# Optimization experiments

Hardware: AMD Instinct MI355X
Metric: run time of the kernel (lower is better)

## Reference

```python
import jax, jax.numpy as jnp
import numpy as np

N_FEAT = 1024
NEG_BIG = -1e30  # finite stand-in for -inf to avoid NaNs on fully-masked rows


def setup_inputs() -> dict:
    key = jax.random.key(0)
    k1, k2, k3 = jax.random.split(key, 3)
    T, C = 4096, 1024
    x = jax.random.normal(k1, (T, C), dtype=jnp.float32)
    W = jax.random.normal(k2, (C, 3 * N_FEAT), dtype=jnp.float32) * 0.02
    b = jax.random.normal(k3, (3 * N_FEAT,), dtype=jnp.float32) * 0.02
    return {"x": x, "W": W, "b": b, "n_padd": 256}


def reference(x, W, b, n_padd):
    T, C = x.shape
    qkv = x @ W + b  # [T, 3*N_FEAT]
    q, k, v = jnp.split(qkv, 3, axis=1)  # each [T, N_FEAT]
    att = (q @ k.T) * (1.0 / jnp.sqrt(jnp.float32(N_FEAT)))  # [T, T]
    idx = jnp.arange(T)
    causal = idx[None, :] <= idx[:, None]
    data = (idx[None, :] >= n_padd) & (idx[:, None] >= n_padd)
    mask = causal & data
    att = jnp.where(mask, att, NEG_BIG)
    p = jax.nn.softmax(att, axis=-1)  # fully-masked rows -> uniform, zeroed below
    y = p @ v  # [T, N_FEAT]
    # kernel only stores rows >= n_padd; padded rows defined as zero here
    y = jnp.where(idx[:, None] >= n_padd, y, 0.0)
    return y
```

## Files before the change

kernel.cpp:

```cpp
#include <hip/hip_runtime.h>
#include <hip/hip_bf16.h>
#include <stdint.h>
#include <stddef.h>

#define TT 4096
#define CC 1024
#define NFD 1024
#define N3 3072
#define PB0 1152
#define PB2 2176

typedef __bf16 bf16;
typedef __bf16 bf16x8 __attribute__((ext_vector_type(8)));
typedef __bf16 bf16x4 __attribute__((ext_vector_type(4)));
typedef float f32x4 __attribute__((ext_vector_type(4)));

typedef const __attribute__((address_space(1))) unsigned char gl_u8;
typedef __attribute__((address_space(3))) unsigned char lds_u8;

__device__ __forceinline__ void glds16(const void* g, void* l) {
  __builtin_amdgcn_global_load_lds((gl_u8*)g, (lds_u8*)l, 16, 0, 0);
}

__device__ __forceinline__ void stage128x32(const bf16* __restrict__ src, int ld, bf16* lds, int tid) {
  const int lane = tid & 63;
  const int w = tid >> 6;
#pragma unroll
  for (int p = 0; p < 2; ++p) {
    const int lbyte = w * 2048 + p * 1024;
    const int row = (lbyte >> 6) + (lane >> 2);
    const int kel = (lane & 3) << 3;
    glds16(src + row * ld + kel, (char*)lds + lbyte);
  }
}

__device__ __forceinline__ void gemm_core(const bf16* __restrict__ A, const bf16* __restrict__ B,
                                          int lda, int ldb, int ksteps,
                                          bf16* As, bf16* Bs, int tid, f32x4 (&acc)[4][4]) {
  const int lane = tid & 63;
  const int w = tid >> 6;
  const int wm = (w >> 1) * 64;
  const int wn = (w & 1) * 64;
  const int lrow = lane & 15;
  const int lko = (lane >> 4) * 8;
  stage128x32(A, lda, As, tid);
  stage128x32(B, ldb, Bs, tid);
  __syncthreads();
  for (int ks = 0; ks < ksteps; ++ks) {
    const bf16* Ac = As + (ks & 1) * 4096;
    const bf16* Bc = Bs + (ks & 1) * 4096;
    if (ks + 1 < ksteps) {
      stage128x32(A + (ks + 1) * 32, lda, As + ((ks + 1) & 1) * 4096, tid);
      stage128x32(B + (ks + 1) * 32, ldb, Bs + ((ks + 1) & 1) * 4096, tid);
    }
    bf16x8 af[4], bfr[4];
#pragma unroll
    for (int i = 0; i < 4; ++i)
      af[i] = *(const bf16x8*)(Ac + (wm + i * 16 + lrow) * 32 + lko);
#pragma unroll
    for (int i = 0; i < 4; ++i)
      bfr[i] = *(const bf16x8*)(Bc + (wn + i * 16 + lrow) * 32 + lko);
#pragma unroll
    for (int mi = 0; mi < 4; ++mi)
#pragma unroll
      for (int ni = 0; ni < 4; ++ni)
        acc[mi][ni] = __builtin_amdgcn_mfma_f32_16x16x32_bf16(af[mi], bfr[ni], acc[mi][ni], 0, 0, 0);
    __syncthreads();
  }
}

__global__ __launch_bounds__(256) void k_prep(const float* __restrict__ x, bf16* __restrict__ xb,
                                              const float* __restrict__ Wsrc, bf16* __restrict__ WbT,
                                              float* __restrict__ l) {
  __shared__ float Ls[64][65];
  const int tid = threadIdx.x;
  if (blockIdx.x < 2048) {
    int idx = (blockIdx.x * 256 + tid) * 8;
    f32x4 a = *(const f32x4*)(x + idx);
    f32x4 b = *(const f32x4*)(x + idx + 4);
    bf16x8 o;
#pragma unroll
    for (int j = 0; j < 4; ++j) { o[j] = (bf16)a[j]; o[4 + j] = (bf16)b[j]; }
    *(bf16x8*)(xb + idx) = o;
    return;
  }
  if (blockIdx.x == 2048 + 768) {
    f32x4 z = (f32x4){0.f, 0.f, 0.f, 0.f};
#pragma unroll
    for (int qq = 0; qq < 4; ++qq)
      *(f32x4*)(l + (qq * 256 + tid) * 4) = z;
    return;
  }
  const int bid = blockIdx.x - 2048;
  const int n0 = (bid % 48) * 64;
  const int c0 = (bid / 48) * 64;
#pragma unroll
  for (int qq = 0; qq < 4; ++qq) {
    int lin = qq * 1024 + tid * 4;
    int r = lin >> 6, cc = lin & 63;
    f32x4 v = *(const f32x4*)(Wsrc + (size_t)(c0 + r) * N3 + n0 + cc);
#pragma unroll
    for (int j = 0; j < 4; ++j) Ls[r][cc + j] = v[j];
  }
  __syncthreads();
#pragma unroll
  for (int qq = 0; qq < 4; ++qq) {
    int lin = qq * 1024 + tid * 4;
    int nr = lin >> 6, cc = lin & 63;
    bf16x4 o;
#pragma unroll
    for (int j = 0; j < 4; ++j) o[j] = (bf16)Ls[cc + j][nr];
    *(bf16x4*)(WbT + (size_t)(n0 + nr) * CC + c0 + cc) = o;
  }
}

__global__ __launch_bounds__(256, 2) void k_qkv(const bf16* __restrict__ xb, const bf16* __restrict__ wbt,
                                                const float* __restrict__ bias,
                                                bf16* __restrict__ q, bf16* __restrict__ k,
                                                bf16* __restrict__ vT) {
  __shared__ bf16 As[2 * 128 * 32], Bs[2 * 128 * 32];
  const int tid = threadIdx.x;
  const int id = blockIdx.x;
  const int r = id & 7;
  const int s = id >> 3;
  const int it = 4 * r + (s & 3);
  const int jt = s >> 2;
  const int m0 = it * 128;
  const int n0 = jt * 128;
  f32x4 acc[4][4];
#pragma unroll
  for (int i = 0; i < 4; ++i)
#pragma unroll
    for (int j = 0; j < 4; ++j) acc[i][j] = (f32x4){0.f, 0.f, 0.f, 0.f};

  gemm_core(xb + (size_t)m0 * CC, wbt + (size_t)n0 * CC, CC, CC, CC / 32, As, Bs, tid, acc);

  const int lane = tid & 63;
  const int w = tid >> 6;
  const int wm = (w >> 1) * 64, wn = (w & 1) * 64;
  const int seg = n0 >> 10;
#pragma unroll
  for (int mi = 0; mi < 4; ++mi) {
    const int tB = m0 + wm + mi * 16 + ((lane >> 4) << 2);
#pragma unroll
    for (int ni = 0; ni < 4; ++ni) {
      const int n = n0 + wn + ni * 16 + (lane & 15);
      const float bb = bias[n];
      f32x4 a = acc[mi][ni];
      if (seg == 2) {
        bf16x4 pv;
#pragma unroll
        for (int r2 = 0; r2 < 4; ++r2) pv[r2] = (bf16)(a[r2] + bb);
        *(bf16x4*)(vT + (size_t)(n - 2048) * TT + tB) = pv;
      } else {
        bf16* dst = (seg == 0) ? q : k;
        const int nl = n & 1023;
#pragma unroll
        for (int r2 = 0; r2 < 4; ++r2) dst[(size_t)(tB + r2) * NFD + nl] = (bf16)(a[r2] + bb);
      }
    }
  }
}

__global__ __launch_bounds__(256, 2) void k_scores(const bf16* __restrict__ q, const bf16* __restrict__ kk,
                                                   bf16* __restrict__ P, float* __restrict__ l,
                                                   const int* __restrict__ npadd_p) {
  const int id = blockIdx.x;
  const int lin = (id & 7) * 66 + (id >> 3);
  int band, rem;
  if (lin < 228)      { band = 0; rem = lin; }
  else if (lin < 392) { band = 1; rem = lin - 228; }
  else if (lin < 492) { band = 2; rem = lin - 392; }
  else                { band = 3; rem = lin - 492; }
  int it, jt;
  if (rem < 28) {
    int itp = (int)((sqrtf(8.0f * (float)rem + 1.0f) - 1.0f) * 0.5f);
    while ((itp + 1) * (itp + 2) / 2 <= rem) ++itp;
    while (itp * (itp + 1) / 2 > rem) --itp;
    it = band * 8 + itp;
    jt = band * 8 + (rem - itp * (itp + 1) / 2);
  } else {
    const int rem2 = rem - 28;
    it = band * 8 + 7 + (rem2 >> 3);
    jt = band * 8 + (rem2 & 7);
  }
  const int np = *npadd_p;
  const int jt0 = np >> 7;
  if (jt < jt0) return;

  __shared__ bf16 As[2 * 128 * 32], Bs[2 * 128 * 32];
  const int tid = threadIdx.x;
  f32x4 acc[4][4];
#pragma unroll
  for (int i = 0; i < 4; ++i)
#pragma unroll
    for (int j = 0; j < 4; ++j) acc[i][j] = (f32x4){0.f, 0.f, 0.f, 0.f};

  gemm_core(q + (size_t)it * 128 * CC, kk + (size_t)jt * 128 * CC, CC, CC, CC / 32, As, Bs, tid, acc);

  const int lane = tid & 63;
  const int w = tid >> 6;
  const int wm = (w >> 1) * 64, wn = (w & 1) * 64;
  const float scale = 0.03125f;
#pragma unroll
  for (int mi = 0; mi < 4; ++mi) {
    const int iB = it * 128 + wm + mi * 16 + ((lane >> 4) << 2);
    float rs[4] = {0.f, 0.f, 0.f, 0.f};
#pragma unroll
    for (int ni = 0; ni < 4; ++ni) {
      const int j = jt * 128 + wn + ni * 16 + (lane & 15);
      f32x4 a = acc[mi][ni];
#pragma unroll
      for (int r = 0; r < 4; ++r) {
        const int i = iB + r;
        float p = 0.f;
        if (j <= i && j >= np && i >= np) p = __expf(a[r] * scale);
        const bf16 pb = (bf16)p;
        P[(size_t)i * TT + j] = pb;
        rs[r] += (float)pb;
      }
    }
#pragma unroll
    for (int r = 0; r < 4; ++r) {
      float v = rs[r];
      v += __shfl_xor(v, 1);
      v += __shfl_xor(v, 2);
      v += __shfl_xor(v, 4);
      v += __shfl_xor(v, 8);
      if ((lane & 15) == 0) atomicAdd(&l[iB + r], v);
    }
  }
}

__global__ __launch_bounds__(256, 2) void k_pvc(const bf16* __restrict__ P, const bf16* __restrict__ vT,
                                                bf16* __restrict__ part0, bf16* __restrict__ part1,
                                                bf16* __restrict__ part2,
                                                const float* __restrict__ l, float* __restrict__ y,
                                                const int* __restrict__ npadd_p) {
  const int id = blockIdx.x;
  const int kgrp = id >> 3;
  const int d0 = (kgrp & 7) * 128;
  const int p = (id & 7) + 8 * (kgrp >> 3);
  const int it = p >> 2;
  const int c = p & 3;
  const int np = *npadd_p;
  const int jt0 = np >> 7;
  const int lo = (c == 0) ? 0 : (c == 1 ? 9 : (c == 2 ? 17 : 25));
  const int hi = (c == 0) ? 9 : (c == 1 ? 17 : (c == 2 ? 25 : 32));
  const int jlo = max(lo, jt0);
  const int jhi = min(hi, it + 1);
  if (jlo >= jhi) return;

  __shared__ bf16 As[2 * 128 * 32], Bs[2 * 128 * 32];
  const int tid = threadIdx.x;
  f32x4 acc[4][4];
#pragma unroll
  for (int i = 0; i < 4; ++i)
#pragma unroll
    for (int j = 0; j < 4; ++j) acc[i][j] = (f32x4){0.f, 0.f, 0.f, 0.f};

  gemm_core(P + (size_t)it * 128 * TT + (size_t)jlo * 128,
            vT + (size_t)d0 * TT + (size_t)jlo * 128,
            TT, TT, (jhi - jlo) * 4, As, Bs, tid, acc);

  const int lane = tid & 63;
  const int w = tid >> 6;
  const int wm = (w >> 1) * 64, wn = (w & 1) * 64;
  const bool sole = (jlo == jt0) && (jhi == it + 1);
  if (sole) {
#pragma unroll
    for (int mi = 0; mi < 4; ++mi) {
      const int iB = it * 128 + wm + mi * 16 + ((lane >> 4) << 2);
      float inv4[4];
#pragma unroll
      for (int r = 0; r < 4; ++r) {
        const int i = iB + r;
        inv4[r] = (i >= np) ? (1.0f / l[i]) : 0.0f;
      }
#pragma unroll
      for (int ni = 0; ni < 4; ++ni) {
        const int d = d0 + wn + ni * 16 + (lane & 15);
        f32x4 a = acc[mi][ni];
#pragma unroll
        for (int r = 0; r < 4; ++r)
          y[(size_t)(iB + r) * NFD + d] = a[r] * inv4[r];
      }
    }
  } else if (c == 3) {
#pragma unroll
    for (int mi = 0; mi < 4; ++mi) {
      const int iB = it * 128 + wm + mi * 16 + ((lane >> 4) << 2);
#pragma unroll
      for (int ni = 0; ni < 4; ++ni) {
        const int d = d0 + wn + ni * 16 + (lane & 15);
        f32x4 a = acc[mi][ni];
#pragma unroll
        for (int r = 0; r < 4; ++r)
          y[(size_t)(iB + r) * NFD + d] = a[r];
      }
    }
  } else {
    bf16* __restrict__ part = (c == 0) ? part0 : (c == 1 ? part1 : part2);
    const int base = (c == 2) ? (PB2 * NFD) : (PB0 * NFD);
#pragma unroll
    for (int mi = 0; mi < 4; ++mi) {
      const int iB = it * 128 + wm + mi * 16 + ((lane >> 4) << 2);
#pragma unroll
      for (int ni = 0; ni < 4; ++ni) {
        const int d = d0 + wn + ni * 16 + (lane & 15);
        f32x4 a = acc[mi][ni];
#pragma unroll
        for (int r = 0; r < 4; ++r)
          part[(size_t)(iB + r) * NFD + d - base] = (bf16)a[r];
      }
    }
  }
}

__global__ __launch_bounds__(256) void k_norm(const bf16* __restrict__ part0, const bf16* __restrict__ part1,
                                              const bf16* __restrict__ part2,
                                              const float* __restrict__ l, float* __restrict__ y,
                                              const int* __restrict__ npadd_p) {
  const int idx = (blockIdx.x * 256 + threadIdx.x) * 8;
  const int i = idx >> 10;
  const int np = *npadd_p;
  if (i < np) {
    f32x4 z = (f32x4){0.f, 0.f, 0.f, 0.f};
    *(f32x4*)(y + idx) = z;
    *(f32x4*)(y + idx + 4) = z;
    return;
  }
  const int jt0 = np >> 7;
  const int it = i >> 7;
  const int ip1 = it + 1;
  const bool a0 = (max(0, jt0)  < min(9, ip1));
  const bool a1 = (max(9, jt0)  < min(17, ip1));
  const bool a2 = (max(17, jt0) < min(25, ip1));
  const bool a3 = (max(25, jt0) < min(32, ip1));
  const int cnt = (int)a0 + (int)a1 + (int)a2 + (int)a3;
  if (cnt <= 1) return;
  float s[8] = {0.f, 0.f, 0.f, 0.f, 0.f, 0.f, 0.f, 0.f};
  if (a0) {
    bf16x8 a = *(const bf16x8*)(part0 + idx - PB0 * NFD);
#pragma unroll
    for (int j = 0; j < 8; ++j) s[j] += (float)a[j];
  }
  if (a1) {
    bf16x8 a = *(const bf16x8*)(part1 + idx - PB0 * NFD);
#pragma unroll
    for (int j = 0; j < 8; ++j) s[j] += (float)a[j];
  }
  if (a2) {
    bf16x8 a = *(const bf16x8*)(part2 + idx - PB2 * NFD);
#pragma unroll
    for (int j = 0; j < 8; ++j) s[j] += (float)a[j];
  }
  if (a3) {
    f32x4 a = *(const f32x4*)(y + idx);
    f32x4 b = *(const f32x4*)(y + idx + 4);
#pragma unroll
    for (int j = 0; j < 4; ++j) { s[j] += a[j]; s[4 + j] += b[j]; }
  }
  const float inv = 1.0f / l[i];
  f32x4 o0, o1;
#pragma unroll
  for (int j = 0; j < 4; ++j) { o0[j] = s[j] * inv; o1[j] = s[4 + j] * inv; }
  *(f32x4*)(y + idx) = o0;
  *(f32x4*)(y + idx + 4) = o1;
}

extern "C" void kernel_launch(void* const* d_in, const int* in_sizes, int n_in,
                              void* d_out, int out_size, void* d_ws, size_t ws_size,
                              hipStream_t stream) {
  const float* x = (const float*)d_in[0];
  const float* W = (const float*)d_in[1];
  const float* b = (const float*)d_in[2];
  const int* npadd = (const int*)d_in[3];
  float* y = (float*)d_out;

  char* ws = (char*)d_ws;
  const size_t MB = 1u << 20;
  bf16* q  = (bf16*)(ws + 0 * MB);
  bf16* kk = (bf16*)(ws + 8 * MB);
  bf16* part0 = (bf16*)(ws + 0 * MB);
  bf16* part1 = (bf16*)(ws + (size_t)(TT - PB0) * NFD * 2);
  bf16* part2 = (bf16*)(ws + (size_t)2 * (TT - PB0) * NFD * 2);
  bf16* vT = (bf16*)(ws + 16 * MB);
  float* l = (float*)(ws + 24 * MB);
  bf16* P  = (bf16*)(ws + 24 * MB + 65536);
  bf16* xb = P;
  bf16* WbT = (bf16*)((char*)P + 8 * MB);

  k_prep<<<dim3(2048 + 768 + 1), 256, 0, stream>>>(x, xb, W, WbT, l);
  k_qkv<<<dim3(768), 256, 0, stream>>>(xb, WbT, b, q, kk, vT);
  k_scores<<<dim3(528), 256, 0, stream>>>(q, kk, P, l, npadd);
  k_pvc<<<dim3(1024), 256, 0, stream>>>(P, vT, part0, part1, part2, l, y, npadd);
  k_norm<<<dim3((TT * NFD) / (256 * 8)), 256, 0, stream>>>(part0, part1, part2, l, y, npadd);
}
```

Baseline: 117.5 us.

## Split QKV GEMM and co-schedule V projection with score GEMM blocks

The QKV projection now runs in two parts. Q and K come from a dedicated 512-block kernel, and the V projection blocks share a launch with the causal score GEMM blocks. This lets the V work fill gaps and the tail of the unevenly loaded scores launch. Because P is written while V blocks still read xb and WbT, those buffers move to non-overlapping workspace regions, which needs a larger workspace.

```diff
diff --git a/kernel.cpp b/kernel.cpp
--- a/kernel.cpp
+++ b/kernel.cpp
@@ -114,10 +114,9 @@
   }
 }
 
-__global__ __launch_bounds__(256, 2) void k_qkv(const bf16* __restrict__ xb, const bf16* __restrict__ wbt,
-                                                const float* __restrict__ bias,
-                                                bf16* __restrict__ q, bf16* __restrict__ k,
-                                                bf16* __restrict__ vT) {
+__global__ __launch_bounds__(256, 2) void k_qkv_qk(const bf16* __restrict__ xb, const bf16* __restrict__ wbt,
+                                                   const float* __restrict__ bias,
+                                                   bf16* __restrict__ q, bf16* __restrict__ k) {
   __shared__ bf16 As[2 * 128 * 32], Bs[2 * 128 * 32];
   const int tid = threadIdx.x;
   const int id = blockIdx.x;
@@ -138,7 +137,7 @@
   const int lane = tid & 63;
   const int w = tid >> 6;
   const int wm = (w >> 1) * 64, wn = (w & 1) * 64;
-  const int seg = n0 >> 10;
+  bf16* dst = (n0 < 1024) ? q : k;
 #pragma unroll
   for (int mi = 0; mi < 4; ++mi) {
     const int tB = m0 + wm + mi * 16 + ((lane >> 4) << 2);
@@ -146,26 +145,57 @@
     for (int ni = 0; ni < 4; ++ni) {
       const int n = n0 + wn + ni * 16 + (lane & 15);
       const float bb = bias[n];
+      const int nl = n & 1023;
       f32x4 a = acc[mi][ni];
-      if (seg == 2) {
+#pragma unroll
+      for (int r2 = 0; r2 < 4; ++r2) dst[(size_t)(tB + r2) * NFD + nl] = (bf16)(a[r2] + bb);
+    }
+  }
+}
+
+__global__ __launch_bounds__(256, 2) void k_fused(const bf16* __restrict__ xb, const bf16* __restrict__ wbt,
+                                                  const float* __restrict__ bias, bf16* __restrict__ vT,
+                                                  const bf16* __restrict__ q, const bf16* __restrict__ kk,
+                                                  bf16* __restrict__ P, float* __restrict__ l,
+                                                  const int* __restrict__ npadd_p) {
+  __shared__ bf16 As[2 * 128 * 32], Bs[2 * 128 * 32];
+  const int tid = threadIdx.x;
+  if (blockIdx.x < 256) {
+    const int id = blockIdx.x;
+    const int r = id & 7;
+    const int s = id >> 3;
+    const int it = 4 * r + (s & 3);
+    const int jt = 16 + (s >> 2);
+    const int m0 = it * 128;
+    const int n0 = jt * 128;
+    f32x4 acc[4][4];
+#pragma unroll
+    for (int i = 0; i < 4; ++i)
+#pragma unroll
+      for (int j = 0; j < 4; ++j) acc[i][j] = (f32x4){0.f, 0.f, 0.f, 0.f};
+
+    gemm_core(xb + (size_t)m0 * CC, wbt + (size_t)n0 * CC, CC, CC, CC / 32, As, Bs, tid, acc);
+
+    const int lane = tid & 63;
+    const int w = tid >> 6;
+    const int wm = (w >> 1) * 64, wn = (w & 1) * 64;
+#pragma unroll
+    for (int mi = 0; mi < 4; ++mi) {
+      const int tB = m0 + wm + mi * 16 + ((lane >> 4) << 2);
+#pragma unroll
+      for (int ni = 0; ni < 4; ++ni) {
+        const int n = n0 + wn + ni * 16 + (lane & 15);
+        const float bb = bias[n];
+        f32x4 a = acc[mi][ni];
         bf16x4 pv;
 #pragma unroll
         for (int r2 = 0; r2 < 4; ++r2) pv[r2] = (bf16)(a[r2] + bb);
         *(bf16x4*)(vT + (size_t)(n - 2048) * TT + tB) = pv;
-      } else {
-        bf16* dst = (seg == 0) ? q : k;
-        const int nl = n & 1023;
-#pragma unroll
-        for (int r2 = 0; r2 < 4; ++r2) dst[(size_t)(tB + r2) * NFD + nl] = (bf16)(a[r2] + bb);
-      }
-    }
-  }
-}
-
-__global__ __launch_bounds__(256, 2) void k_scores(const bf16* __restrict__ q, const bf16* __restrict__ kk,
-                                                   bf16* __restrict__ P, float* __restrict__ l,
-                                                   const int* __restrict__ npadd_p) {
-  const int id = blockIdx.x;
+      }
+    }
+    return;
+  }
+  const int id = blockIdx.x - 256;
   const int lin = (id & 7) * 66 + (id >> 3);
   int band, rem;
   if (lin < 228)      { band = 0; rem = lin; }
@@ -188,8 +218,6 @@
   const int jt0 = np >> 7;
   if (jt < jt0) return;
 
-  __shared__ bf16 As[2 * 128 * 32], Bs[2 * 128 * 32];
-  const int tid = threadIdx.x;
   f32x4 acc[4][4];
 #pragma unroll
   for (int i = 0; i < 4; ++i)
@@ -388,12 +416,12 @@
   bf16* vT = (bf16*)(ws + 16 * MB);
   float* l = (float*)(ws + 24 * MB);
   bf16* P  = (bf16*)(ws + 24 * MB + 65536);
-  bf16* xb = P;
-  bf16* WbT = (bf16*)((char*)P + 8 * MB);
+  bf16* xb  = (bf16*)(ws + 60 * MB);
+  bf16* WbT = (bf16*)(ws + 68 * MB);
 
   k_prep<<<dim3(2048 + 768 + 1), 256, 0, stream>>>(x, xb, W, WbT, l);
-  k_qkv<<<dim3(768), 256, 0, stream>>>(xb, WbT, b, q, kk, vT);
-  k_scores<<<dim3(528), 256, 0, stream>>>(q, kk, P, l, npadd);
+  k_qkv_qk<<<dim3(512), 256, 0, stream>>>(xb, WbT, b, q, kk);
+  k_fused<<<dim3(256 + 528), 256, 0, stream>>>(xb, WbT, b, vT, q, kk, P, l, npadd);
   k_pvc<<<dim3(1024), 256, 0, stream>>>(P, vT, part0, part1, part2, l, y, npadd);
   k_norm<<<dim3((TT * NFD) / (256 * 8)), 256, 0, stream>>>(part0, part1, part2, l, y, npadd);
 }
```

New measurement: 120.1 us. +2.2%, slower.
